# Kernel tuning notes

Measured on AMD Instinct MI355X. Metric: run time of the kernel, lower is better.

## Reference

```python
import jax, jax.numpy as jnp
import numpy as np

N_W, N_D = 50000, 20000
E_WW, E_WD = 500000, 300000
IN, HID, OUT = 256, 128, 128


def _glorot(key, shape):
    fan_in, fan_out = shape
    s = (2.0 / (fan_in + fan_out)) ** 0.5
    return jax.random.normal(key, shape, dtype=jnp.float32) * s


def setup_inputs() -> dict:
    key = jax.random.key(0)
    ks = jax.random.split(key, 32)
    d = {}
    d['x_word'] = jax.random.normal(ks[0], (N_W, IN), dtype=jnp.float32)
    d['x_doc'] = jax.random.normal(ks[1], (N_D, IN), dtype=jnp.float32)
    # edge lists per relation (src, dst)
    d['src_ww'] = jax.random.randint(ks[2], (E_WW,), 0, N_W, dtype=jnp.int32)
    d['dst_ww'] = jax.random.randint(ks[3], (E_WW,), 0, N_W, dtype=jnp.int32)
    d['src_wd'] = jax.random.randint(ks[4], (E_WD,), 0, N_W, dtype=jnp.int32)
    d['dst_wd'] = jax.random.randint(ks[5], (E_WD,), 0, N_D, dtype=jnp.int32)
    d['src_wwr'] = jax.random.randint(ks[6], (E_WW,), 0, N_W, dtype=jnp.int32)
    d['dst_wwr'] = jax.random.randint(ks[7], (E_WW,), 0, N_W, dtype=jnp.int32)
    d['src_dwr'] = jax.random.randint(ks[8], (E_WD,), 0, N_D, dtype=jnp.int32)
    d['dst_dwr'] = jax.random.randint(ks[9], (E_WD,), 0, N_W, dtype=jnp.int32)
    # per-layer, per-relation GraphConv weights and biases
    dims = [(IN, HID), (HID, OUT)]
    i = 10
    for layer in (1, 2):
        shp = dims[layer - 1]
        for rel in ('ww', 'wd', 'wwr', 'dwr'):
            d[f'W{layer}_{rel}'] = _glorot(ks[i], shp); i += 1
            d[f'b{layer}_{rel}'] = jnp.zeros((shp[1],), jnp.float32)
    d['lin_w'] = _glorot(ks[i], (OUT, 1))
    d['lin_b'] = jnp.ones((1,), jnp.float32)
    return d


def _gconv(x_src, W, b, src, dst, n_src, n_dst):
    # DGL GraphConv, norm='both': D_dst^{-1/2} A D_src^{-1/2} X W + b
    ones = jnp.ones(src.shape[0], x_src.dtype)
    deg_o = jnp.clip(jax.ops.segment_sum(ones, src, num_segments=n_src), 1.0)
    deg_i = jnp.clip(jax.ops.segment_sum(ones, dst, num_segments=n_dst), 1.0)
    h = (x_src * jax.lax.rsqrt(deg_o)[:, None]) @ W  # weight first (in >= out)
    agg = jax.ops.segment_sum(h[src], dst, num_segments=n_dst)  # [n_dst, out]
    return agg * jax.lax.rsqrt(deg_i)[:, None] + b


def reference(x_word, x_doc,
              src_ww, dst_ww, src_wd, dst_wd, src_wwr, dst_wwr, src_dwr, dst_dwr,
              W1_ww, b1_ww, W1_wd, b1_wd, W1_wwr, b1_wwr, W1_dwr, b1_dwr,
              W2_ww, b2_ww, W2_wd, b2_wd, W2_wwr, b2_wwr, W2_dwr, b2_dwr,
              lin_w, lin_b):
    def layer(xw, xd, W_ww, b_ww, W_wd, b_wd, W_wwr, b_wwr, W_dwr, b_dwr):
        # 'word' dst: stack over 3 relations then sum == sum of contributions
        w_new = (_gconv(xw, W_ww, b_ww, src_ww, dst_ww, N_W, N_W)
                 + _gconv(xw, W_wwr, b_wwr, src_wwr, dst_wwr, N_W, N_W)
                 + _gconv(xd, W_dwr, b_dwr, src_dwr, dst_dwr, N_D, N_W))
        d_new = _gconv(xw, W_wd, b_wd, src_wd, dst_wd, N_W, N_D)
        return jax.nn.relu(w_new), jax.nn.relu(d_new)

    xw, xd = layer(x_word, x_doc, W1_ww, b1_ww, W1_wd, b1_wd, W1_wwr, b1_wwr, W1_dwr, b1_dwr)
    xw, xd = layer(xw, xd, W2_ww, b2_ww, W2_wd, b2_wd, W2_wwr, b2_wwr, W2_dwr, b2_dwr)
    out_w = jax.nn.sigmoid(xw @ lin_w + lin_b)  # [N_W, 1]
    out_d = jax.nn.sigmoid(xd @ lin_w + lin_b)  # [N_D, 1]
    return out_w, out_d
```

## Files before the change

kernel.cpp:

```cpp
#include <hip/hip_runtime.h>
#include <hip/hip_bf16.h>


#define N_W 50000
#define N_D 20000
#define E_WW 500000
#define E_WD 300000
#define NTOT 170000

#define C_WW 40
#define C_WD 48
#define C_DWR 32

#define NB_WW 196
#define NB_WD 79
#define NB_DWR 196
#define CAPB_WW 2816
#define CAPB_WD 4096
#define CAPB_DWR 1792

#define NBS_W 196
#define NBS_D 79
#define CAPS_WW 2816
#define CAPS_WD 1792
#define CAPS_DWR 4352

typedef __attribute__((ext_vector_type(8))) short short8;
typedef __attribute__((ext_vector_type(4))) float f32x4;

static __device__ __forceinline__ unsigned f2bf_u(float x) {
  unsigned u = __float_as_uint(x);
  return (u + 0x7fff + ((u >> 16) & 1)) >> 16;
}
static __device__ __forceinline__ unsigned short f2bf(float x) {
  return (unsigned short)f2bf_u(x);
}
static __device__ __forceinline__ float bf2f(unsigned short b) {
  return __uint_as_float((unsigned)b << 16);
}
static __device__ __forceinline__ void gld16(const void* g, void* l) {
  __builtin_amdgcn_global_load_lds(
      (const __attribute__((address_space(1))) void*)g,
      (__attribute__((address_space(3))) void*)l, 16, 0, 0);
}

struct Args {
  const float *x_word, *x_doc;
  const int *src_ww, *dst_ww, *src_wd, *dst_wd, *src_wwr, *dst_wwr, *src_dwr, *dst_dwr;
  const float *W1_ww, *W1_wd, *W1_wwr, *W1_dwr;
  const float *W2_ww, *W2_wd, *W2_wwr, *W2_dwr;
  const float *b1_ww, *b1_wd, *b1_wwr, *b1_dwr;
  const float *b2_ww, *b2_wd, *b2_wwr, *b2_dwr;
  const float *lin_w, *lin_b;
  float *out;
  int *cnt256d;
  int *cnt256s;
  int *cur;
  float *degF;
  unsigned short *csr_ww, *csr_wwr, *csr_wd, *csr_dwr;
  unsigned int *stg_ww, *stg_wwr, *stg_wd, *stg_dwr;
  unsigned char *sst_ww, *sst_wwr, *sst_wd, *sst_dwr;
  unsigned short *xw_bf, *xd_bf, *h_w3, *h_d, *Bt1w, *Bt1d, *Bt2w, *Bt2d;
  unsigned short *accW1, *accD1;
};

#define BS_WW 123
#define BS_WD 74
#define BV_W 12500
#define BV_D 5000
#define BP1W 384
#define BP1D 128
#define BP2W 192
#define BP2D 64
#define BG_W 391
#define BG_D 157
#define BGR_W 6250
#define BGR_D 2500

static __device__ __forceinline__ void lds_scan256(int* cnt, int* bas, int* scn) {
  const int t = threadIdx.x;
  scn[t] = cnt[t];
  __syncthreads();
#pragma unroll
  for (int off = 1; off < 256; off <<= 1) {
    int v = (t >= off) ? scn[t - off] : 0;
    __syncthreads();
    scn[t] += v;
    __syncthreads();
  }
  bas[t] = scn[t] - cnt[t];
  scn[t] = bas[t];
  __syncthreads();
}

static __device__ void dev_pass1(
    const int* __restrict__ src, const int* __restrict__ dst, int E,
    unsigned int* __restrict__ stageD, int CAPBD, int* __restrict__ cntD,
    unsigned char* __restrict__ stageS, int CAPBS, int* __restrict__ cntS,
    int lb, int* cnt, int* bas, int* scn, unsigned int* lstage) {
  const int t = threadIdx.x;
  const int eb = lb * 4096;
  unsigned int w[16];
  cnt[t] = 0;
  __syncthreads();
#pragma unroll
  for (int u = 0; u < 16; u++) {
    int e = eb + u * 256 + t;
    if (e < E) {
      int s = src[e], d = dst[e];
      w[u] = ((unsigned)s << 16) | (unsigned)d;
      atomicAdd(&cnt[d >> 8], 1);
    } else {
      w[u] = 0xFFFFFFFFu;
    }
  }
  __syncthreads();
  lds_scan256(cnt, bas, scn);
#pragma unroll
  for (int u = 0; u < 16; u++) {
    if (w[u] != 0xFFFFFFFFu) {
      int bk = (w[u] & 0xFFFFu) >> 8;
      int p = atomicAdd(&scn[bk], 1);
      lstage[p] = w[u];
    }
  }
  __syncthreads();
  {
    int n = cnt[t];
    if (n > 0) {
      int g = atomicAdd(&cntD[t], n);
      unsigned int* dp = stageD + (size_t)t * CAPBD + g;
      int lb2 = bas[t];
      for (int k = 0; k < n; k++)
        if (g + k < CAPBD) dp[k] = lstage[lb2 + k];
    }
  }
  __syncthreads();
  cnt[t] = 0;
  __syncthreads();
#pragma unroll
  for (int u = 0; u < 16; u++)
    if (w[u] != 0xFFFFFFFFu) atomicAdd(&cnt[w[u] >> 24], 1);
  __syncthreads();
  lds_scan256(cnt, bas, scn);
  unsigned char* lbytes = (unsigned char*)lstage;
#pragma unroll
  for (int u = 0; u < 16; u++) {
    if (w[u] != 0xFFFFFFFFu) {
      int bk = w[u] >> 24;
      int p = atomicAdd(&scn[bk], 1);
      lbytes[p] = (unsigned char)((w[u] >> 16) & 0xFF);
    }
  }
  __syncthreads();
  {
    int n = cnt[t];
    if (n > 0) {
      int g = atomicAdd(&cntS[t], n);
      unsigned char* dp = stageS + (size_t)t * CAPBS + g;
      int lb2 = bas[t];
      for (int k = 0; k < n; k++)
        if (g + k < CAPBS) dp[k] = lbytes[lb2 + k];
    }
  }
}

static __device__ __forceinline__ void dev_cvt(
    const float* __restrict__ x, unsigned short* __restrict__ y, int i, int n4) {
  if (i < n4) {
    float4 v = ((const float4*)x)[i];
    ushort4 u;
    u.x = f2bf(v.x); u.y = f2bf(v.y); u.z = f2bf(v.z); u.w = f2bf(v.w);
    ((ushort4*)y)[i] = u;
  }
}
static __device__ __forceinline__ void dev_packB(
    const float* __restrict__ W0, const float* __restrict__ W1,
    const float* __restrict__ W2, int kshift, int total, int i,
    unsigned short* __restrict__ out) {
  if (i >= total) return;
  int n = i >> kshift, k = i & ((1 << kshift) - 1);
  const float* W = (n < 128) ? W0 : ((n < 256) ? W1 : W2);
  out[i] = f2bf(W[(size_t)k * 128 + (n & 127)]);
}

__global__ __launch_bounds__(256) void prep1_kernel(Args a) {
  __shared__ int cnt[256], bas[256], scn[256];
  __shared__ unsigned int lstage[4096];
  int b = blockIdx.x;
  const int t = threadIdx.x;
  if (b < BS_WW) { dev_pass1(a.src_ww, a.dst_ww, E_WW, a.stg_ww, CAPB_WW, a.cnt256d, a.sst_ww, CAPS_WW, a.cnt256s, b, cnt, bas, scn, lstage); return; }
  b -= BS_WW;
  if (b < BS_WW) { dev_pass1(a.src_wwr, a.dst_wwr, E_WW, a.stg_wwr, CAPB_WW, a.cnt256d + 256, a.sst_wwr, CAPS_WW, a.cnt256s + 256, b, cnt, bas, scn, lstage); return; }
  b -= BS_WW;
  if (b < BS_WD) { dev_pass1(a.src_wd, a.dst_wd, E_WD, a.stg_wd, CAPB_WD, a.cnt256d + 512, a.sst_wd, CAPS_WD, a.cnt256s + 512, b, cnt, bas, scn, lstage); return; }
  b -= BS_WD;
  if (b < BS_WD) { dev_pass1(a.src_dwr, a.dst_dwr, E_WD, a.stg_dwr, CAPB_DWR, a.cnt256d + 768, a.sst_dwr, CAPS_DWR, a.cnt256s + 768, b, cnt, bas, scn, lstage); return; }
  b -= BS_WD;
  if (b < BV_W) { dev_cvt(a.x_word, a.xw_bf, b * 256 + t, N_W * 64); return; }
  b -= BV_W;
  if (b < BV_D) { dev_cvt(a.x_doc, a.xd_bf, b * 256 + t, N_D * 64); return; }
  b -= BV_D;
  if (b < BP1W) { dev_packB(a.W1_ww, a.W1_wwr, a.W1_wd, 8, 384 * 256, b * 256 + t, a.Bt1w); return; }
  b -= BP1W;
  if (b < BP1D) { dev_packB(a.W1_dwr, a.W1_dwr, a.W1_dwr, 8, 128 * 256, b * 256 + t, a.Bt1d); return; }
  b -= BP1D;
  if (b < BP2W) { dev_packB(a.W2_ww, a.W2_wwr, a.W2_wd, 7, 384 * 128, b * 256 + t, a.Bt2w); return; }
  b -= BP2W;
  dev_packB(a.W2_dwr, a.W2_dwr, a.W2_dwr, 7, 128 * 128, b * 256 + t, a.Bt2d);
}

static __device__ void dev_pass2(
    const unsigned int* __restrict__ stage, int CAPB, int C, int Nrel,
    const int* __restrict__ cntD, int* __restrict__ curRel,
    unsigned short* __restrict__ csr, int b,
    int* cnt2, unsigned short* slice) {
  const int t = threadIdx.x;
  cnt2[t] = 0;
  __syncthreads();
  int n = cntD[b];
  if (n > CAPB) n = CAPB;
  const unsigned int* sp = stage + (size_t)b * CAPB;
  for (int e = t; e < n; e += 256) {
    unsigned int w = sp[e];
    int dl = w & 0xFF;
    int s = w >> 16;
    int p = atomicAdd(&cnt2[dl], 1);
    if (p < C) slice[dl * C + p] = (unsigned short)s;
  }
  __syncthreads();
  const int words = 256 * C / 2;
  unsigned int* g32 = (unsigned int*)csr + (size_t)b * (128 * C);
  const unsigned int* s32 = (const unsigned int*)slice;
  for (int i = t; i < words; i += 256) g32[i] = s32[i];
  int node = b * 256 + t;
  if (node < Nrel) curRel[node] = cnt2[t];
}

static __device__ void dev_pass2b(
    const unsigned char* __restrict__ stage, int CAPB, int Nrel,
    const int* __restrict__ cntS, float* __restrict__ degFRel, int b,
    int* cnt2) {
  const int t = threadIdx.x;
  cnt2[t] = 0;
  __syncthreads();
  int n = cntS[b];
  if (n > CAPB) n = CAPB;
  const unsigned char* sp = stage + (size_t)b * CAPB;
  for (int e = t; e < n; e += 256) atomicAdd(&cnt2[sp[e]], 1);
  __syncthreads();
  int node = b * 256 + t;
  if (node < Nrel) degFRel[node] = rsqrtf(fmaxf((float)cnt2[t], 1.0f));
}

__global__ __launch_bounds__(256) void pass2_kernel(Args a) {
  __shared__ int cnt2[256];
  __shared__ unsigned short slice[256 * 48];
  int b = blockIdx.x;
  if (b < NB_WW) { dev_pass2(a.stg_ww, CAPB_WW, C_WW, N_W, a.cnt256d, a.cur, a.csr_ww, b, cnt2, slice); return; }
  b -= NB_WW;
  if (b < NB_WW) { dev_pass2(a.stg_wwr, CAPB_WW, C_WW, N_W, a.cnt256d + 256, a.cur + 50000, a.csr_wwr, b, cnt2, slice); return; }
  b -= NB_WW;
  if (b < NB_WD) { dev_pass2(a.stg_wd, CAPB_WD, C_WD, N_D, a.cnt256d + 512, a.cur + 100000, a.csr_wd, b, cnt2, slice); return; }
  b -= NB_WD;
  if (b < NB_DWR) { dev_pass2(a.stg_dwr, CAPB_DWR, C_DWR, N_W, a.cnt256d + 768, a.cur + 120000, a.csr_dwr, b, cnt2, slice); return; }
  b -= NB_DWR;
  if (b < NBS_W) { dev_pass2b(a.sst_ww, CAPS_WW, N_W, a.cnt256s, a.degF, b, cnt2); return; }
  b -= NBS_W;
  if (b < NBS_W) { dev_pass2b(a.sst_wwr, CAPS_WW, N_W, a.cnt256s + 256, a.degF + 50000, b, cnt2); return; }
  b -= NBS_W;
  if (b < NBS_W) { dev_pass2b(a.sst_wd, CAPS_WD, N_W, a.cnt256s + 512, a.degF + 100000, b, cnt2); return; }
  b -= NBS_W;
  dev_pass2b(a.sst_dwr, CAPS_DWR, N_D, a.cnt256s + 768, a.degF + 150000, b, cnt2);
}

template <int K>
static __device__ void dev_gemm(
    const unsigned short* __restrict__ A, int M,
    const unsigned short* __restrict__ BtSub,
    const float* __restrict__ degF,
    unsigned short* __restrict__ C, int cstride, int coloff,
    int bx, unsigned char* smem) {
  const int row0 = bx * 128;
  const int tid = threadIdx.x;
  const int lane = tid & 63;
  const int wave = tid >> 6;
  const int wr = wave >> 1;
  const int wc = wave & 1;
  const int lc = lane & 15;
  const int quad = lane >> 4;

  unsigned char* sA = smem;
  unsigned char* sB = smem + 16384;
  const int mn = tid & 127;
  const int kc0 = tid >> 7;
  const unsigned short* arow = A + (size_t)(row0 + mn) * K;
  const unsigned short* brow = BtSub + (size_t)mn * K;
  unsigned char* ldsA = sA + wave * 1024;
  unsigned char* ldsB = sB + wave * 1024;

  f32x4 acc[4][4];
#pragma unroll
  for (int p = 0; p < 4; p++)
#pragma unroll
    for (int q = 0; q < 4; q++) acc[p][q] = {0.f, 0.f, 0.f, 0.f};

  for (int k0 = 0; k0 < K; k0 += 64) {
#pragma unroll
    for (int i = 0; i < 4; i++) {
      int kk = k0 + (i * 2 + kc0) * 8;
      gld16(arow + kk, ldsA + i * 4096);
      gld16(brow + kk, ldsB + i * 4096);
    }
    __syncthreads();
#pragma unroll
    for (int s = 0; s < 2; s++) {
      const int ko = (s * 4 + quad) * 2048 + lc * 16;
      short8 av[4], bv[4];
#pragma unroll
      for (int p = 0; p < 4; p++)
        av[p] = *(const short8*)(sA + ko + (wr * 64 + p * 16) * 16);
#pragma unroll
      for (int q = 0; q < 4; q++)
        bv[q] = *(const short8*)(sB + ko + (wc * 64 + q * 16) * 16);
#pragma unroll
      for (int p = 0; p < 4; p++)
#pragma unroll
        for (int q = 0; q < 4; q++)
          acc[p][q] = __builtin_amdgcn_mfma_f32_16x16x32_bf16(
              av[p], bv[q], acc[p][q], 0, 0, 0);
    }
    __syncthreads();
  }

  const int colb = coloff + wc * 64;
#pragma unroll
  for (int p = 0; p < 4; p++) {
#pragma unroll
    for (int i = 0; i < 4; i++) {
      int r = row0 + wr * 64 + p * 16 + quad * 4 + i;
      if (r >= M) continue;
      float sc = degF[r];
      unsigned short* cp = C + (size_t)r * cstride + colb + lc;
#pragma unroll
      for (int q = 0; q < 4; q++) cp[q * 16] = f2bf(acc[p][q][i] * sc);
    }
  }
}

__global__ __launch_bounds__(256) void gemm1_kernel(Args a) {
  __shared__ __align__(16) unsigned char smem[32768];
  int b = blockIdx.x;
  if (b < BG_W) { dev_gemm<256>(a.xw_bf, N_W, a.Bt1w,                     a.degF,          a.h_w3, 384, 0,   b, smem); return; }
  b -= BG_W;
  if (b < BG_W) { dev_gemm<256>(a.xw_bf, N_W, a.Bt1w + (size_t)128 * 256, a.degF + 50000,  a.h_w3, 384, 128, b, smem); return; }
  b -= BG_W;
  if (b < BG_W) { dev_gemm<256>(a.xw_bf, N_W, a.Bt1w + (size_t)256 * 256, a.degF + 100000, a.h_w3, 384, 256, b, smem); return; }
  b -= BG_W;
  dev_gemm<256>(a.xd_bf, N_D, a.Bt1d, a.degF + 150000, a.h_d, 128, 0, b, smem);
}

__global__ __launch_bounds__(256) void gemm2_kernel(Args a) {
  __shared__ __align__(16) unsigned char smem[32768];
  int b = blockIdx.x;
  if (b < BG_W) { dev_gemm<128>(a.accW1, N_W, a.Bt2w,                     a.degF,          a.h_w3, 384, 0,   b, smem); return; }
  b -= BG_W;
  if (b < BG_W) { dev_gemm<128>(a.accW1, N_W, a.Bt2w + (size_t)128 * 128, a.degF + 50000,  a.h_w3, 384, 128, b, smem); return; }
  b -= BG_W;
  if (b < BG_W) { dev_gemm<128>(a.accW1, N_W, a.Bt2w + (size_t)256 * 128, a.degF + 100000, a.h_w3, 384, 256, b, smem); return; }
  b -= BG_W;
  dev_gemm<128>(a.accD1, N_D, a.Bt2d, a.degF + 150000, a.h_d, 128, 0, b, smem);
}

static __device__ __forceinline__ float4 edge_sum32(
    const unsigned short* __restrict__ base, int stride,
    const unsigned short* __restrict__ csr, int st, int en, int lane32) {
  float4 s0 = make_float4(0.f, 0.f, 0.f, 0.f);
  float4 s1 = make_float4(0.f, 0.f, 0.f, 0.f);
  float4 s2 = make_float4(0.f, 0.f, 0.f, 0.f);
  float4 s3 = make_float4(0.f, 0.f, 0.f, 0.f);
  for (int b = st; b < en; b += 32) {
    int n = en - b; if (n > 32) n = 32;
    int t = b + lane32;
    int idx = csr[t < en ? t : en - 1];
    int j = 0;
    for (; j + 3 < n; j += 4) {
      int e0 = __shfl(idx, j, 32), e1 = __shfl(idx, j + 1, 32);
      int e2 = __shfl(idx, j + 2, 32), e3 = __shfl(idx, j + 3, 32);
      ushort4 u0 = *(const ushort4*)(base + (size_t)e0 * stride);
      ushort4 u1 = *(const ushort4*)(base + (size_t)e1 * stride);
      ushort4 u2 = *(const ushort4*)(base + (size_t)e2 * stride);
      ushort4 u3 = *(const ushort4*)(base + (size_t)e3 * stride);
      s0.x += bf2f(u0.x); s0.y += bf2f(u0.y); s0.z += bf2f(u0.z); s0.w += bf2f(u0.w);
      s1.x += bf2f(u1.x); s1.y += bf2f(u1.y); s1.z += bf2f(u1.z); s1.w += bf2f(u1.w);
      s2.x += bf2f(u2.x); s2.y += bf2f(u2.y); s2.z += bf2f(u2.z); s2.w += bf2f(u2.w);
      s3.x += bf2f(u3.x); s3.y += bf2f(u3.y); s3.z += bf2f(u3.z); s3.w += bf2f(u3.w);
    }
    for (; j < n; j++) {
      int e0 = __shfl(idx, j, 32);
      ushort4 u0 = *(const ushort4*)(base + (size_t)e0 * stride);
      s0.x += bf2f(u0.x); s0.y += bf2f(u0.y); s0.z += bf2f(u0.z); s0.w += bf2f(u0.w);
    }
  }
  return make_float4(s0.x + s1.x + s2.x + s3.x, s0.y + s1.y + s2.y + s3.y,
                     s0.z + s1.z + s2.z + s3.z, s0.w + s1.w + s2.w + s3.w);
}

template <int HEAD>
__global__ __launch_bounds__(256) void gather_kernel(Args a) {
  const int lane32 = threadIdx.x & 31;
  const int f = lane32 * 4;
  int blk = blockIdx.x;
  float v[4];
  float* outp;
  unsigned short* accp;

  if (blk < BGR_W) {
    int g = blk * 8 + (threadIdx.x >> 5);
    int c1 = a.cur[g];
    int c2 = a.cur[50000 + g];
    int c3 = a.cur[120000 + g];
    int l1 = c1 < C_WW ? c1 : C_WW;
    int l2 = c2 < C_WW ? c2 : C_WW;
    int l3 = c3 < C_DWR ? c3 : C_DWR;
    float4 s1 = edge_sum32(a.h_w3 + f, 384, a.csr_ww, g * C_WW, g * C_WW + l1, lane32);
    float4 s2 = edge_sum32(a.h_w3 + 128 + f, 384, a.csr_wwr, g * C_WW, g * C_WW + l2, lane32);
    float4 s3 = edge_sum32(a.h_d + f, 128, a.csr_dwr, g * C_DWR, g * C_DWR + l3, lane32);
    float r1 = rsqrtf(fmaxf((float)c1, 1.f));
    float r2 = rsqrtf(fmaxf((float)c2, 1.f));
    float r3 = rsqrtf(fmaxf((float)c3, 1.f));
    const float* b0 = HEAD ? a.b2_ww : a.b1_ww;
    const float* b1 = HEAD ? a.b2_wwr : a.b1_wwr;
    const float* b2 = HEAD ? a.b2_dwr : a.b1_dwr;
#pragma unroll
    for (int i = 0; i < 4; i++) {
      float bb = b0[f + i] + b1[f + i] + b2[f + i];
      v[i] = fmaxf((&s1.x)[i] * r1 + (&s2.x)[i] * r2 + (&s3.x)[i] * r3 + bb, 0.f);
    }
    outp = a.out + g;
    accp = a.accW1 + (size_t)g * 128 + f;
  } else {
    int g = (blk - BGR_W) * 8 + (threadIdx.x >> 5);
    int c1 = a.cur[100000 + g];
    int l1 = c1 < C_WD ? c1 : C_WD;
    float4 s1 = edge_sum32(a.h_w3 + 256 + f, 384, a.csr_wd, g * C_WD, g * C_WD + l1, lane32);
    float r1 = rsqrtf(fmaxf((float)c1, 1.f));
    const float* b0 = HEAD ? a.b2_wd : a.b1_wd;
#pragma unroll
    for (int i = 0; i < 4; i++)
      v[i] = fmaxf((&s1.x)[i] * r1 + b0[f + i], 0.f);
    outp = a.out + N_W + g;
    accp = a.accD1 + (size_t)g * 128 + f;
  }

  if (HEAD) {
    float4 w4 = *(const float4*)(a.lin_w + f);
    float p = v[0] * w4.x + v[1] * w4.y + v[2] * w4.z + v[3] * w4.w;
#pragma unroll
    for (int off = 16; off > 0; off >>= 1) p += __shfl_down(p, off, 32);
    if (lane32 == 0) *outp = 1.0f / (1.0f + expf(-(p + a.lin_b[0])));
  } else {
    ushort4 o;
    o.x = f2bf(v[0]); o.y = f2bf(v[1]); o.z = f2bf(v[2]); o.w = f2bf(v[3]);
    *(ushort4*)accp = o;
  }
}

extern "C" void kernel_launch(void* const* d_in, const int* in_sizes, int n_in,
                              void* d_out, int out_size, void* d_ws, size_t ws_size,
                              hipStream_t stream) {
  Args a;
  a.x_word = (const float*)d_in[0];
  a.x_doc  = (const float*)d_in[1];
  a.src_ww  = (const int*)d_in[2];
  a.dst_ww  = (const int*)d_in[3];
  a.src_wd  = (const int*)d_in[4];
  a.dst_wd  = (const int*)d_in[5];
  a.src_wwr = (const int*)d_in[6];
  a.dst_wwr = (const int*)d_in[7];
  a.src_dwr = (const int*)d_in[8];
  a.dst_dwr = (const int*)d_in[9];
  a.W1_ww  = (const float*)d_in[10]; a.b1_ww  = (const float*)d_in[11];
  a.W1_wd  = (const float*)d_in[12]; a.b1_wd  = (const float*)d_in[13];
  a.W1_wwr = (const float*)d_in[14]; a.b1_wwr = (const float*)d_in[15];
  a.W1_dwr = (const float*)d_in[16]; a.b1_dwr = (const float*)d_in[17];
  a.W2_ww  = (const float*)d_in[18]; a.b2_ww  = (const float*)d_in[19];
  a.W2_wd  = (const float*)d_in[20]; a.b2_wd  = (const float*)d_in[21];
  a.W2_wwr = (const float*)d_in[22]; a.b2_wwr = (const float*)d_in[23];
  a.W2_dwr = (const float*)d_in[24]; a.b2_dwr = (const float*)d_in[25];
  a.lin_w  = (const float*)d_in[26];
  a.lin_b  = (const float*)d_in[27];
  a.out = (float*)d_out;

  char* ws = (char*)d_ws;
  size_t off = 0;
  auto alloc = [&](size_t n4) { void* p = ws + off * 4; off += n4; return p; };
  a.cnt256d = (int*)alloc(1024);
  a.cnt256s = (int*)alloc(1024);
  const size_t zero4 = off;
  a.cur  = (int*)alloc(NTOT);
  a.degF = (float*)alloc(NTOT);
  a.csr_ww  = (unsigned short*)alloc((size_t)NB_WW * 256 * C_WW / 2);
  a.csr_wwr = (unsigned short*)alloc((size_t)NB_WW * 256 * C_WW / 2);
  a.csr_wd  = (unsigned short*)alloc((size_t)NB_WD * 256 * C_WD / 2);
  a.csr_dwr = (unsigned short*)alloc((size_t)NB_DWR * 256 * C_DWR / 2);
  a.xw_bf = (unsigned short*)alloc((size_t)N_W * 256 / 2);
  a.xd_bf = (unsigned short*)alloc((size_t)N_D * 256 / 2);
  a.h_w3  = (unsigned short*)alloc((size_t)N_W * 384 / 2);
  a.h_d   = (unsigned short*)alloc((size_t)N_D * 128 / 2);
  a.Bt1w  = (unsigned short*)alloc(384 * 256 / 2);
  a.Bt1d  = (unsigned short*)alloc(128 * 256 / 2);
  a.Bt2w  = (unsigned short*)alloc(384 * 128 / 2);
  a.Bt2d  = (unsigned short*)alloc(128 * 128 / 2);
  a.accW1 = a.xw_bf;
  a.accD1 = a.xw_bf + (size_t)N_W * 128;
  unsigned int* stg = (unsigned int*)a.h_w3;
  a.stg_ww  = stg;  stg += (size_t)NB_WW * CAPB_WW;
  a.stg_wwr = stg;  stg += (size_t)NB_WW * CAPB_WW;
  a.stg_wd  = stg;  stg += (size_t)NB_WD * CAPB_WD;
  a.stg_dwr = stg;  stg += (size_t)NB_DWR * CAPB_DWR;
  unsigned char* sstg = (unsigned char*)stg;
  a.sst_ww  = sstg; sstg += (size_t)NBS_W * CAPS_WW;
  a.sst_wwr = sstg; sstg += (size_t)NBS_W * CAPS_WW;
  a.sst_wd  = sstg; sstg += (size_t)NBS_W * CAPS_WD;
  a.sst_dwr = sstg;
  (void)ws_size;

  hipMemsetAsync(d_ws, 0, zero4 * 4, stream);

  prep1_kernel<<<2 * BS_WW + 2 * BS_WD + BV_W + BV_D + BP1W + BP1D + BP2W + BP2D,
                 256, 0, stream>>>(a);
  pass2_kernel<<<2 * NB_WW + NB_WD + NB_DWR + 3 * NBS_W + NBS_D, 256, 0, stream>>>(a);
  gemm1_kernel<<<3 * BG_W + BG_D, 256, 0, stream>>>(a);
  gather_kernel<0><<<BGR_W + BGR_D, 256, 0, stream>>>(a);
  gemm2_kernel<<<3 * BG_W + BG_D, 256, 0, stream>>>(a);
  gather_kernel<1><<<BGR_W + BGR_D, 256, 0, stream>>>(a);
}
```

Before: 374.2 us.

## Merge CSR pass2 with layer-1 GEMM by moving source-degree scaling into gather

```diff
diff --git a/kernel.cpp b/kernel.cpp
--- a/kernel.cpp
+++ b/kernel.cpp
@@ -253,32 +253,10 @@
   if (node < Nrel) degFRel[node] = rsqrtf(fmaxf((float)cnt2[t], 1.0f));
 }
 
-__global__ __launch_bounds__(256) void pass2_kernel(Args a) {
-  __shared__ int cnt2[256];
-  __shared__ unsigned short slice[256 * 48];
-  int b = blockIdx.x;
-  if (b < NB_WW) { dev_pass2(a.stg_ww, CAPB_WW, C_WW, N_W, a.cnt256d, a.cur, a.csr_ww, b, cnt2, slice); return; }
-  b -= NB_WW;
-  if (b < NB_WW) { dev_pass2(a.stg_wwr, CAPB_WW, C_WW, N_W, a.cnt256d + 256, a.cur + 50000, a.csr_wwr, b, cnt2, slice); return; }
-  b -= NB_WW;
-  if (b < NB_WD) { dev_pass2(a.stg_wd, CAPB_WD, C_WD, N_D, a.cnt256d + 512, a.cur + 100000, a.csr_wd, b, cnt2, slice); return; }
-  b -= NB_WD;
-  if (b < NB_DWR) { dev_pass2(a.stg_dwr, CAPB_DWR, C_DWR, N_W, a.cnt256d + 768, a.cur + 120000, a.csr_dwr, b, cnt2, slice); return; }
-  b -= NB_DWR;
-  if (b < NBS_W) { dev_pass2b(a.sst_ww, CAPS_WW, N_W, a.cnt256s, a.degF, b, cnt2); return; }
-  b -= NBS_W;
-  if (b < NBS_W) { dev_pass2b(a.sst_wwr, CAPS_WW, N_W, a.cnt256s + 256, a.degF + 50000, b, cnt2); return; }
-  b -= NBS_W;
-  if (b < NBS_W) { dev_pass2b(a.sst_wd, CAPS_WD, N_W, a.cnt256s + 512, a.degF + 100000, b, cnt2); return; }
-  b -= NBS_W;
-  dev_pass2b(a.sst_dwr, CAPS_DWR, N_D, a.cnt256s + 768, a.degF + 150000, b, cnt2);
-}
-
 template <int K>
 static __device__ void dev_gemm(
     const unsigned short* __restrict__ A, int M,
     const unsigned short* __restrict__ BtSub,
-    const float* __restrict__ degF,
     unsigned short* __restrict__ C, int cstride, int coloff,
     int bx, unsigned char* smem) {
   const int row0 = bx * 128;
@@ -340,41 +318,58 @@
     for (int i = 0; i < 4; i++) {
       int r = row0 + wr * 64 + p * 16 + quad * 4 + i;
       if (r >= M) continue;
-      float sc = degF[r];
       unsigned short* cp = C + (size_t)r * cstride + colb + lc;
 #pragma unroll
-      for (int q = 0; q < 4; q++) cp[q * 16] = f2bf(acc[p][q][i] * sc);
-    }
-  }
-}
-
-__global__ __launch_bounds__(256) void gemm1_kernel(Args a) {
+      for (int q = 0; q < 4; q++) cp[q * 16] = f2bf(acc[p][q][i]);
+    }
+  }
+}
+
+__global__ __launch_bounds__(256) void mid_kernel(Args a) {
   __shared__ __align__(16) unsigned char smem[32768];
+  __shared__ int cnt2[256];
   int b = blockIdx.x;
-  if (b < BG_W) { dev_gemm<256>(a.xw_bf, N_W, a.Bt1w,                     a.degF,          a.h_w3, 384, 0,   b, smem); return; }
+  if (b < NB_WW) { dev_pass2(a.stg_ww, CAPB_WW, C_WW, N_W, a.cnt256d, a.cur, a.csr_ww, b, cnt2, (unsigned short*)smem); return; }
+  b -= NB_WW;
+  if (b < NB_WW) { dev_pass2(a.stg_wwr, CAPB_WW, C_WW, N_W, a.cnt256d + 256, a.cur + 50000, a.csr_wwr, b, cnt2, (unsigned short*)smem); return; }
+  b -= NB_WW;
+  if (b < NB_WD) { dev_pass2(a.stg_wd, CAPB_WD, C_WD, N_D, a.cnt256d + 512, a.cur + 100000, a.csr_wd, b, cnt2, (unsigned short*)smem); return; }
+  b -= NB_WD;
+  if (b < NB_DWR) { dev_pass2(a.stg_dwr, CAPB_DWR, C_DWR, N_W, a.cnt256d + 768, a.cur + 120000, a.csr_dwr, b, cnt2, (unsigned short*)smem); return; }
+  b -= NB_DWR;
+  if (b < NBS_W) { dev_pass2b(a.sst_ww, CAPS_WW, N_W, a.cnt256s, a.degF, b, cnt2); return; }
+  b -= NBS_W;
+  if (b < NBS_W) { dev_pass2b(a.sst_wwr, CAPS_WW, N_W, a.cnt256s + 256, a.degF + 50000, b, cnt2); return; }
+  b -= NBS_W;
+  if (b < NBS_W) { dev_pass2b(a.sst_wd, CAPS_WD, N_W, a.cnt256s + 512, a.degF + 100000, b, cnt2); return; }
+  b -= NBS_W;
+  if (b < NBS_D) { dev_pass2b(a.sst_dwr, CAPS_DWR, N_D, a.cnt256s + 768, a.degF + 150000, b, cnt2); return; }
+  b -= NBS_D;
+  if (b < BG_W) { dev_gemm<256>(a.xw_bf, N_W, a.Bt1w,                     a.h_w3, 384, 0,   b, smem); return; }
   b -= BG_W;
-  if (b < BG_W) { dev_gemm<256>(a.xw_bf, N_W, a.Bt1w + (size_t)128 * 256, a.degF + 50000,  a.h_w3, 384, 128, b, smem); return; }
+  if (b < BG_W) { dev_gemm<256>(a.xw_bf, N_W, a.Bt1w + (size_t)128 * 256, a.h_w3, 384, 128, b, smem); return; }
   b -= BG_W;
-  if (b < BG_W) { dev_gemm<256>(a.xw_bf, N_W, a.Bt1w + (size_t)256 * 256, a.degF + 100000, a.h_w3, 384, 256, b, smem); return; }
+  if (b < BG_W) { dev_gemm<256>(a.xw_bf, N_W, a.Bt1w + (size_t)256 * 256, a.h_w3, 384, 256, b, smem); return; }
   b -= BG_W;
-  dev_gemm<256>(a.xd_bf, N_D, a.Bt1d, a.degF + 150000, a.h_d, 128, 0, b, smem);
+  dev_gemm<256>(a.xd_bf, N_D, a.Bt1d, a.h_d, 128, 0, b, smem);
 }
 
 __global__ __launch_bounds__(256) void gemm2_kernel(Args a) {
   __shared__ __align__(16) unsigned char smem[32768];
   int b = blockIdx.x;
-  if (b < BG_W) { dev_gemm<128>(a.accW1, N_W, a.Bt2w,                     a.degF,          a.h_w3, 384, 0,   b, smem); return; }
+  if (b < BG_W) { dev_gemm<128>(a.accW1, N_W, a.Bt2w,                     a.h_w3, 384, 0,   b, smem); return; }
   b -= BG_W;
-  if (b < BG_W) { dev_gemm<128>(a.accW1, N_W, a.Bt2w + (size_t)128 * 128, a.degF + 50000,  a.h_w3, 384, 128, b, smem); return; }
+  if (b < BG_W) { dev_gemm<128>(a.accW1, N_W, a.Bt2w + (size_t)128 * 128, a.h_w3, 384, 128, b, smem); return; }
   b -= BG_W;
-  if (b < BG_W) { dev_gemm<128>(a.accW1, N_W, a.Bt2w + (size_t)256 * 128, a.degF + 100000, a.h_w3, 384, 256, b, smem); return; }
+  if (b < BG_W) { dev_gemm<128>(a.accW1, N_W, a.Bt2w + (size_t)256 * 128, a.h_w3, 384, 256, b, smem); return; }
   b -= BG_W;
-  dev_gemm<128>(a.accD1, N_D, a.Bt2d, a.degF + 150000, a.h_d, 128, 0, b, smem);
+  dev_gemm<128>(a.accD1, N_D, a.Bt2d, a.h_d, 128, 0, b, smem);
 }
 
 static __device__ __forceinline__ float4 edge_sum32(
     const unsigned short* __restrict__ base, int stride,
-    const unsigned short* __restrict__ csr, int st, int en, int lane32) {
+    const unsigned short* __restrict__ csr, const float* __restrict__ degF,
+    int st, int en, int lane32) {
   float4 s0 = make_float4(0.f, 0.f, 0.f, 0.f);
   float4 s1 = make_float4(0.f, 0.f, 0.f, 0.f);
   float4 s2 = make_float4(0.f, 0.f, 0.f, 0.f);
@@ -387,19 +382,21 @@
     for (; j + 3 < n; j += 4) {
       int e0 = __shfl(idx, j, 32), e1 = __shfl(idx, j + 1, 32);
       int e2 = __shfl(idx, j + 2, 32), e3 = __shfl(idx, j + 3, 32);
+      float f0 = degF[e0], f1 = degF[e1], f2 = degF[e2], f3 = degF[e3];
       ushort4 u0 = *(const ushort4*)(base + (size_t)e0 * stride);
       ushort4 u1 = *(const ushort4*)(base + (size_t)e1 * stride);
       ushort4 u2 = *(const ushort4*)(base + (size_t)e2 * stride);
       ushort4 u3 = *(const ushort4*)(base + (size_t)e3 * stride);
-      s0.x += bf2f(u0.x); s0.y += bf2f(u0.y); s0.z += bf2f(u0.z); s0.w += bf2f(u0.w);
-      s1.x += bf2f(u1.x); s1.y += bf2f(u1.y); s1.z += bf2f(u1.z); s1.w += bf2f(u1.w);
-      s2.x += bf2f(u2.x); s2.y += bf2f(u2.y); s2.z += bf2f(u2.z); s2.w += bf2f(u2.w);
-      s3.x += bf2f(u3.x); s3.y += bf2f(u3.y); s3.z += bf2f(u3.z); s3.w += bf2f(u3.w);
+      s0.x += bf2f(u0.x) * f0; s0.y += bf2f(u0.y) * f0; s0.z += bf2f(u0.z) * f0; s0.w += bf2f(u0.w) * f0;
+      s1.x += bf2f(u1.x) * f1; s1.y += bf2f(u1.y) * f1; s1.z += bf2f(u1.z) * f1; s1.w += bf2f(u1.w) * f1;
+      s2.x += bf2f(u2.x) * f2; s2.y += bf2f(u2.y) * f2; s2.z += bf2f(u2.z) * f2; s2.w += bf2f(u2.w) * f2;
+      s3.x += bf2f(u3.x) * f3; s3.y += bf2f(u3.y) * f3; s3.z += bf2f(u3.z) * f3; s3.w += bf2f(u3.w) * f3;
     }
     for (; j < n; j++) {
       int e0 = __shfl(idx, j, 32);
+      float f0 = degF[e0];
       ushort4 u0 = *(const ushort4*)(base + (size_t)e0 * stride);
-      s0.x += bf2f(u0.x); s0.y += bf2f(u0.y); s0.z += bf2f(u0.z); s0.w += bf2f(u0.w);
+      s0.x += bf2f(u0.x) * f0; s0.y += bf2f(u0.y) * f0; s0.z += bf2f(u0.z) * f0; s0.w += bf2f(u0.w) * f0;
     }
   }
   return make_float4(s0.x + s1.x + s2.x + s3.x, s0.y + s1.y + s2.y + s3.y,
@@ -423,9 +420,9 @@
     int l1 = c1 < C_WW ? c1 : C_WW;
     int l2 = c2 < C_WW ? c2 : C_WW;
     int l3 = c3 < C_DWR ? c3 : C_DWR;
-    float4 s1 = edge_sum32(a.h_w3 + f, 384, a.csr_ww, g * C_WW, g * C_WW + l1, lane32);
-    float4 s2 = edge_sum32(a.h_w3 + 128 + f, 384, a.csr_wwr, g * C_WW, g * C_WW + l2, lane32);
-    float4 s3 = edge_sum32(a.h_d + f, 128, a.csr_dwr, g * C_DWR, g * C_DWR + l3, lane32);
+    float4 s1 = edge_sum32(a.h_w3 + f, 384, a.csr_ww, a.degF, g * C_WW, g * C_WW + l1, lane32);
+    float4 s2 = edge_sum32(a.h_w3 + 128 + f, 384, a.csr_wwr, a.degF + 50000, g * C_WW, g * C_WW + l2, lane32);
+    float4 s3 = edge_sum32(a.h_d + f, 128, a.csr_dwr, a.degF + 150000, g * C_DWR, g * C_DWR + l3, lane32);
     float r1 = rsqrtf(fmaxf((float)c1, 1.f));
     float r2 = rsqrtf(fmaxf((float)c2, 1.f));
     float r3 = rsqrtf(fmaxf((float)c3, 1.f));
@@ -443,7 +440,7 @@
     int g = (blk - BGR_W) * 8 + (threadIdx.x >> 5);
     int c1 = a.cur[100000 + g];
     int l1 = c1 < C_WD ? c1 : C_WD;
-    float4 s1 = edge_sum32(a.h_w3 + 256 + f, 384, a.csr_wd, g * C_WD, g * C_WD + l1, lane32);
+    float4 s1 = edge_sum32(a.h_w3 + 256 + f, 384, a.csr_wd, a.degF + 100000, g * C_WD, g * C_WD + l1, lane32);
     float r1 = rsqrtf(fmaxf((float)c1, 1.f));
     const float* b0 = HEAD ? a.b2_wd : a.b1_wd;
 #pragma unroll
@@ -514,12 +511,12 @@
   a.Bt2d  = (unsigned short*)alloc(128 * 128 / 2);
   a.accW1 = a.xw_bf;
   a.accD1 = a.xw_bf + (size_t)N_W * 128;
-  unsigned int* stg = (unsigned int*)a.h_w3;
+  unsigned int* stg = (unsigned int*)alloc((size_t)(2 * NB_WW * CAPB_WW + NB_WD * CAPB_WD + NB_DWR * CAPB_DWR));
   a.stg_ww  = stg;  stg += (size_t)NB_WW * CAPB_WW;
   a.stg_wwr = stg;  stg += (size_t)NB_WW * CAPB_WW;
   a.stg_wd  = stg;  stg += (size_t)NB_WD * CAPB_WD;
-  a.stg_dwr = stg;  stg += (size_t)NB_DWR * CAPB_DWR;
-  unsigned char* sstg = (unsigned char*)stg;
+  a.stg_dwr = stg;
+  unsigned char* sstg = (unsigned char*)alloc((NBS_W * (2 * CAPS_WW + CAPS_WD) + NBS_D * CAPS_DWR + 3) / 4);
   a.sst_ww  = sstg; sstg += (size_t)NBS_W * CAPS_WW;
   a.sst_wwr = sstg; sstg += (size_t)NBS_W * CAPS_WW;
   a.sst_wd  = sstg; sstg += (size_t)NBS_W * CAPS_WD;
@@ -530,8 +527,8 @@
 
   prep1_kernel<<<2 * BS_WW + 2 * BS_WD + BV_W + BV_D + BP1W + BP1D + BP2W + BP2D,
                  256, 0, stream>>>(a);
-  pass2_kernel<<<2 * NB_WW + NB_WD + NB_DWR + 3 * NBS_W + NBS_D, 256, 0, stream>>>(a);
-  gemm1_kernel<<<3 * BG_W + BG_D, 256, 0, stream>>>(a);
+  mid_kernel<<<2 * NB_WW + NB_WD + NB_DWR + 3 * NBS_W + NBS_D + 3 * BG_W + BG_D,
+               256, 0, stream>>>(a);
   gather_kernel<0><<<BGR_W + BGR_D, 256, 0, stream>>>(a);
   gemm2_kernel<<<3 * BG_W + BG_D, 256, 0, stream>>>(a);
   gather_kernel<1><<<BGR_W + BGR_D, 256, 0, stream>>>(a);
```

Result: no change. 380.2 us (+1.6%).
